# Kernel tuning notes

Measured on AMD Instinct MI355X. Metric: run time of the kernel, lower is better.

The kernel has to match this reference:

```python
import jax, jax.numpy as jnp
import numpy as np

L, H, HM, E = 2, 1024, 256, 64  # layers, hidden, hyper hidden, hyper embedding
B, T, D = 64, 256, 1024         # batch, time, input size (D == H so layers stack)


def setup_inputs() -> dict:
    key = jax.random.key(0)
    ks = jax.random.split(key, 16)
    n = jax.random.normal
    inp = {
        'x':   n(ks[0], (B, T, D), jnp.float32),
        # main LSTM weights: 4 gates (i,f,g,o); last dim is the input dim
        'Wx':  n(ks[1], (L, 4, H, D), jnp.float32) / np.sqrt(D),
        'Wh':  n(ks[2], (L, 4, H, H), jnp.float32) / np.sqrt(H),
        # hyper (meta) LSTM: input is concat(x_t, h) of size D+H
        'Wmx': n(ks[3], (L, 4 * HM, D + H), jnp.float32) / np.sqrt(D + H),
        'Wmh': n(ks[4], (L, 4 * HM, HM), jnp.float32) / np.sqrt(HM),
        'bm':  jnp.zeros((L, 4 * HM), jnp.float32),
        # hyper embeddings z per gate (hidden->4xE projections)
        'Wzx': n(ks[5], (L, HM, 4, E), jnp.float32) / np.sqrt(HM),
        'bzx': jnp.ones((L, 4, E), jnp.float32),
        'Wzh': n(ks[6], (L, HM, 4, E), jnp.float32) / np.sqrt(HM),
        'bzh': jnp.ones((L, 4, E), jnp.float32),
        'Wzb': n(ks[7], (L, HM, 4, E), jnp.float32) / np.sqrt(HM),
        # embedding -> per-unit modulation (E->H per gate)
        'Px':  n(ks[8], (L, 4, E, H), jnp.float32) / np.sqrt(E),
        'Ph':  n(ks[9], (L, 4, E, H), jnp.float32) / np.sqrt(E),
        'Pb':  n(ks[10], (L, 4, E, H), jnp.float32) / np.sqrt(E),
    }
    return inp


def _meta_lstm_forward(x, Wx, Wh, Wmx, Wmh, bm, Wzx, bzx, Wzh, bzh, Wzb, Px, Ph, Pb):
    Bb = x.shape[0]
    inp = x
    for l in range(L):
        def step(carry, xt, l=l):
            h, c, mh, mc = carry
            # hyper LSTM step on concat(x_t, h)
            xcat = jnp.concatenate([xt, h], axis=-1)
            mpre = xcat @ Wmx[l].T + mh @ Wmh[l].T + bm[l]
            mi, mf, mg, mo = jnp.split(mpre, 4, axis=-1)
            mc2 = jax.nn.sigmoid(mf) * mc + jax.nn.sigmoid(mi) * jnp.tanh(mg)
            mh2 = jax.nn.sigmoid(mo) * jnp.tanh(mc2)
            # gate embeddings and per-unit modulation vectors [B,4,H]
            zx = jnp.einsum('bm,mge->bge', mh2, Wzx[l]) + bzx[l]
            zh = jnp.einsum('bm,mge->bge', mh2, Wzh[l]) + bzh[l]
            zb = jnp.einsum('bm,mge->bge', mh2, Wzb[l])
            dx = jnp.einsum('bge,geh->bgh', zx, Px[l])
            dh = jnp.einsum('bge,geh->bgh', zh, Ph[l])
            db = jnp.einsum('bge,geh->bgh', zb, Pb[l])
            # main LSTM gate pre-activations, hyper-modulated
            gx = jnp.einsum('bd,ghd->bgh', xt, Wx[l])
            gh = jnp.einsum('bk,ghk->bgh', h, Wh[l])
            pre = dx * gx + dh * gh + db
            i_, f_, g_, o_ = pre[:, 0], pre[:, 1], pre[:, 2], pre[:, 3]
            c2 = jax.nn.sigmoid(f_) * c + jax.nn.sigmoid(i_) * jnp.tanh(g_)
            h2 = jax.nn.sigmoid(o_) * jnp.tanh(c2)
            return (h2, c2, mh2, mc2), h2
        init = (jnp.zeros((Bb, H), x.dtype), jnp.zeros((Bb, H), x.dtype),
                jnp.zeros((Bb, HM), x.dtype), jnp.zeros((Bb, HM), x.dtype))
        xs = jnp.swapaxes(inp, 0, 1)  # [T,B,D]
        _, hs = jax.lax.scan(step, init, xs)
        inp = jnp.swapaxes(hs, 0, 1)  # [B,T,H]
    return inp


def reference(x, Wx, Wh, Wmx, Wmh, bm, Wzx, bzx, Wzh, bzh, Wzb, Px, Ph, Pb):
    return _meta_lstm_forward(x, Wx, Wh, Wmx, Wmh, bm, Wzx, bzx, Wzh, bzh, Wzb, Px, Ph, Pb)
```

## Files before the change

kernel.cpp:

```cpp
#include <hip/hip_runtime.h>

#define Bb 64
#define Tt 256
#define Dd 1024
#define Hh 1024
#define HMm 256
#define Ee 64
#define DH 2048

__device__ __forceinline__ float b2f(unsigned short u){
    union{unsigned int i; float f;} v; v.i = ((unsigned int)u) << 16; return v.f;
}
__device__ __forceinline__ unsigned short f2bf(float f){
    union{float f; unsigned int i;} v; v.f = f;
    unsigned int x = v.i;
    unsigned int r = (x + 0x7fffu + ((x >> 16) & 1u)) >> 16;
    return (unsigned short)r;
}
__device__ __forceinline__ void up2(unsigned int u, float& lo, float& hi){
    union{unsigned int i; float f;} x, y;
    x.i = u << 16; y.i = u & 0xffff0000u; lo = x.f; hi = y.f;
}
__device__ __forceinline__ float sigf(float x){ return 1.f/(1.f + expf(-x)); }

__device__ __forceinline__ float dotT(const unsigned short* a, const unsigned short* w, float acc){
    uint4 ua = *(const uint4*)(const void*)a;
    uint4 uw = *(const uint4*)(const void*)w;
    float a0,a1,b0,b1;
    up2(ua.x,a0,a1); up2(uw.x,b0,b1); acc += a0*b0; acc += a1*b1;
    up2(ua.y,a0,a1); up2(uw.y,b0,b1); acc += a0*b0; acc += a1*b1;
    up2(ua.z,a0,a1); up2(uw.z,b0,b1); acc += a0*b0; acc += a1*b1;
    up2(ua.w,a0,a1); up2(uw.w,b0,b1); acc += a0*b0; acc += a1*b1;
    return acc;
}
__device__ __forceinline__ float dotT(const float* a, const unsigned short* w, float acc){
    float4 f0 = *(const float4*)(const void*)a;
    float4 f1 = *(const float4*)(const void*)(a+4);
    uint4 uw = *(const uint4*)(const void*)w;
    float b0,b1;
    up2(uw.x,b0,b1); acc += f0.x*b0; acc += f0.y*b1;
    up2(uw.y,b0,b1); acc += f0.z*b0; acc += f0.w*b1;
    up2(uw.z,b0,b1); acc += f1.x*b0; acc += f1.y*b1;
    up2(uw.w,b0,b1); acc += f1.z*b0; acc += f1.w*b1;
    return acc;
}
__device__ __forceinline__ float dotT(const float* a, const float* w, float acc){
    float4 a0 = *(const float4*)(const void*)a;
    float4 a1 = *(const float4*)(const void*)(a+4);
    float4 w0 = *(const float4*)(const void*)w;
    float4 w1 = *(const float4*)(const void*)(w+4);
    acc += a0.x*w0.x; acc += a0.y*w0.y; acc += a0.z*w0.z; acc += a0.w*w0.w;
    acc += a1.x*w1.x; acc += a1.y*w1.y; acc += a1.z*w1.z; acc += a1.w*w1.w;
    return acc;
}
__device__ __forceinline__ float ldT(const unsigned short* p){ return b2f(*p); }
__device__ __forceinline__ float ldT(const float* p){ return *p; }
__device__ __forceinline__ void stT(unsigned short* p, float v){ *p = f2bf(v); }
__device__ __forceinline__ void stT(float* p, float v){ *p = v; }

__global__ void k_detect(const unsigned short* __restrict__ x, int* __restrict__ flag){
    int tid = threadIdx.x;
    float v = fabsf(b2f(x[2 * tid]));
    bool in = (v > 1e-4f) && (v < 50.f);
    unsigned long long m = __ballot(in);
    if(tid == 0) *flag = (__popcll(m) >= 32) ? 0 : 1;
}

template<typename T>
__global__ __launch_bounds__(256) void k_meta(
    const T* __restrict__ xseq, int t,
    const float* __restrict__ hprev,
    const float* __restrict__ mhprev,
    float* __restrict__ mhnext,
    float* __restrict__ mc,
    const T* __restrict__ Wmx,
    const T* __restrict__ Wmh,
    const T* __restrict__ bm,
    float* __restrict__ xbuf,
    const int* __restrict__ flag)
{
    if(*flag != (int)(sizeof(T) == 4)) return;
    int tid = threadIdx.x;
    {
        int gid = blockIdx.x * 256 + tid;
        int xb = gid >> 10, xd = gid & 1023;
        xbuf[gid] = ldT(&xseq[((size_t)xb * Tt + t) * Dd + xd]);
    }
    int g  = tid & 3;
    int jj = (tid >> 2) & 3;
    int bb = tid >> 4;
    int j  = (blockIdx.x & 63) * 4 + jj;
    int b  = (blockIdx.x >> 6) * 16 + bb;
    int row = g * HMm + j;
    const T* xr  = xseq + ((size_t)b * Tt + t) * Dd;
    const T* wr  = Wmx + (size_t)row * DH;
    const T* wr2 = wr + Dd;
    const T* wm  = Wmh + (size_t)row * HMm;
    const float* hr = hprev + b * Hh;
    const float* mr = mhprev + b * HMm;
    float a0 = ldT(&bm[row]), a1 = 0.f, a2 = 0.f, a3 = 0.f;
    for(int d = 0; d < Dd; d += 32){
        a0 = dotT(xr+d,    wr+d,    a0);
        a1 = dotT(xr+d+8,  wr+d+8,  a1);
        a2 = dotT(xr+d+16, wr+d+16, a2);
        a3 = dotT(xr+d+24, wr+d+24, a3);
    }
    for(int k = 0; k < Hh; k += 32){
        a0 = dotT(hr+k,    wr2+k,    a0);
        a1 = dotT(hr+k+8,  wr2+k+8,  a1);
        a2 = dotT(hr+k+16, wr2+k+16, a2);
        a3 = dotT(hr+k+24, wr2+k+24, a3);
    }
    for(int m = 0; m < HMm; m += 32){
        a0 = dotT(mr+m,    wm+m,    a0);
        a1 = dotT(mr+m+8,  wm+m+8,  a1);
        a2 = dotT(mr+m+16, wm+m+16, a2);
        a3 = dotT(mr+m+24, wm+m+24, a3);
    }
    __shared__ float s[256];
    s[tid] = (a0 + a1) + (a2 + a3);
    __syncthreads();
    if(g == 0){
        float mi = s[tid], mf = s[tid+1], mg = s[tid+2], mo = s[tid+3];
        int idx = b * HMm + j;
        float mc2 = sigf(mf) * mc[idx] + sigf(mi) * tanhf(mg);
        mc[idx] = mc2;
        mhnext[idx] = sigf(mo) * tanhf(mc2);
    }
}

template<typename T>
__global__ __launch_bounds__(256) void k_z(
    const float* __restrict__ mh,
    const T* __restrict__ Wzx,
    const T* __restrict__ Wzh,
    const T* __restrict__ Wzb,
    const T* __restrict__ bzx,
    const T* __restrict__ bzh,
    float* __restrict__ z,
    const int* __restrict__ flag)
{
    if(*flag != (int)(sizeof(T) == 4)) return;
    int col = threadIdx.x;
    int b = blockIdx.x & 63;
    int s = blockIdx.x >> 6;
    const T* W = (s == 0) ? Wzx : ((s == 1) ? Wzh : Wzb);
    float acc = (s == 0) ? ldT(&bzx[col]) : ((s == 1) ? ldT(&bzh[col]) : 0.f);
    const float* mr = mh + b * HMm;
    #pragma unroll 8
    for(int m = 0; m < HMm; m++)
        acc += mr[m] * ldT(&W[m * 256 + col]);
    z[(size_t)(s * Bb + b) * 256 + col] = acc;
}

template<typename T>
__global__ __launch_bounds__(256) void k_main(
    const float* __restrict__ xbuf, int t,
    const float* __restrict__ hprev,
    float* __restrict__ hnext,
    float* __restrict__ c,
    const float* __restrict__ z,
    const T* __restrict__ Px,
    const T* __restrict__ Ph,
    const T* __restrict__ Pb,
    const T* __restrict__ Wx,
    const T* __restrict__ Wh,
    T* __restrict__ oseq,
    const int* __restrict__ flag)
{
    if(*flag != (int)(sizeof(T) == 4)) return;
    int tid = threadIdx.x;
    int hh = tid & 15, bb = tid >> 4;
    int h = (blockIdx.x & 63) * 16 + hh;
    int b = (blockIdx.x >> 6) * 16 + bb;
    const float* xr = xbuf + (size_t)b * Dd;
    const float* hr = hprev + b * Hh;
    const float* zxr = z + (size_t)b * 256;
    const float* zhr = z + (size_t)(Bb + b) * 256;
    const float* zbr = z + (size_t)(2 * Bb + b) * 256;
    float pre[4];
    #pragma unroll
    for(int g = 0; g < 4; g++){
        const T* wxr = Wx + ((size_t)g * Hh + h) * Dd;
        const T* whr = Wh + ((size_t)g * Hh + h) * Hh;
        float x0 = 0.f, x1 = 0.f, h0 = 0.f, h1 = 0.f;
        for(int d = 0; d < Dd; d += 16){
            x0 = dotT(xr+d,   wxr+d,   x0);
            x1 = dotT(xr+d+8, wxr+d+8, x1);
        }
        for(int k = 0; k < Hh; k += 16){
            h0 = dotT(hr+k,   whr+k,   h0);
            h1 = dotT(hr+k+8, whr+k+8, h1);
        }
        float gx = x0 + x1, gh = h0 + h1;
        const float* zx = zxr + g * Ee;
        const float* zh = zhr + g * Ee;
        const float* zb = zbr + g * Ee;
        float dx = 0.f, dh = 0.f, db = 0.f;
        #pragma unroll 8
        for(int e = 0; e < Ee; e++){
            int pi = (g * Ee + e) * Hh + h;
            dx += zx[e] * ldT(&Px[pi]);
            dh += zh[e] * ldT(&Ph[pi]);
            db += zb[e] * ldT(&Pb[pi]);
        }
        pre[g] = dx * gx + dh * gh + db;
    }
    int idx = b * Hh + h;
    float c2 = sigf(pre[1]) * c[idx] + sigf(pre[0]) * tanhf(pre[2]);
    float h2 = sigf(pre[3]) * tanhf(c2);
    c[idx] = c2;
    hnext[idx] = h2;
    stT(&oseq[((size_t)b * Tt + t) * Hh + h], h2);
}

#define LP(Ty, base, off) ((const Ty*)(base) + (off))

extern "C" void kernel_launch(void* const* d_in, const int* in_sizes, int n_in,
                              void* d_out, int out_size, void* d_ws, size_t ws_size,
                              hipStream_t stream) {
    (void)in_sizes; (void)n_in; (void)out_size; (void)ws_size;
    float* ws   = (float*)d_ws;
    float* h0   = ws;
    float* h1   = h0 + 65536;
    float* c    = h1 + 65536;
    float* mh0  = c  + 65536;
    float* mh1  = mh0 + 16384;
    float* mc   = mh1 + 16384;
    float* z    = mc  + 16384;
    float* xbuf = z   + 49152;
    int*   flag = (int*)(xbuf + 65536);

    k_detect<<<1, 64, 0, stream>>>((const unsigned short*)d_in[0], flag);

    for(int l = 0; l < 2; l++){
        hipMemsetAsync(ws, 0, (size_t)(3 * 65536 + 3 * 16384) * sizeof(float), stream);
        size_t oWx  = (size_t)l * 4 * Hh * Dd;
        size_t oWh  = (size_t)l * 4 * Hh * Hh;
        size_t oWmx = (size_t)l * 1024 * DH;
        size_t oWmh = (size_t)l * 1024 * HMm;
        size_t obm  = (size_t)l * 1024;
        size_t oWz  = (size_t)l * HMm * 256;
        size_t obz  = (size_t)l * 256;
        size_t oP   = (size_t)l * 4 * Ee * Hh;

        float *hp = h0, *hn = h1, *mp = mh0, *mn = mh1;
        for(int t = 0; t < Tt; t++){
            k_meta<unsigned short><<<256, 256, 0, stream>>>(
                LP(unsigned short, d_in[0], 0), t, hp, mp, mn, mc,
                LP(unsigned short, d_in[3], oWmx), LP(unsigned short, d_in[4], oWmh),
                LP(unsigned short, d_in[5], obm), xbuf, flag);
            k_meta<float><<<256, 256, 0, stream>>>(
                LP(float, d_in[0], 0), t, hp, mp, mn, mc,
                LP(float, d_in[3], oWmx), LP(float, d_in[4], oWmh),
                LP(float, d_in[5], obm), xbuf, flag);

            k_z<unsigned short><<<192, 256, 0, stream>>>(
                mn, LP(unsigned short, d_in[6], oWz), LP(unsigned short, d_in[8], oWz),
                LP(unsigned short, d_in[10], oWz), LP(unsigned short, d_in[7], obz),
                LP(unsigned short, d_in[9], obz), z, flag);
            k_z<float><<<192, 256, 0, stream>>>(
                mn, LP(float, d_in[6], oWz), LP(float, d_in[8], oWz),
                LP(float, d_in[10], oWz), LP(float, d_in[7], obz),
                LP(float, d_in[9], obz), z, flag);

            void* ov = (l == 0) ? (void*)d_in[0] : d_out;
            k_main<unsigned short><<<256, 256, 0, stream>>>(
                xbuf, t, hp, hn, c, z,
                LP(unsigned short, d_in[11], oP), LP(unsigned short, d_in[12], oP),
                LP(unsigned short, d_in[13], oP), LP(unsigned short, d_in[1], oWx),
                LP(unsigned short, d_in[2], oWh), (unsigned short*)ov, flag);
            k_main<float><<<256, 256, 0, stream>>>(
                xbuf, t, hp, hn, c, z,
                LP(float, d_in[11], oP), LP(float, d_in[12], oP),
                LP(float, d_in[13], oP), LP(float, d_in[1], oWx),
                LP(float, d_in[2], oWh), (float*)ov, flag);

            float* tmp = hp; hp = hn; hn = tmp;
            tmp = mp; mp = mn; mn = tmp;
        }
    }
}
```

Measured before the change: 244.4 ms.

## Fuse per-timestep kernels into one persistent cooperative kernel with grid syncs

Replaces the three per-timestep kernel launches (meta LSTM, z projection, main LSTM), each doubled for two dtype paths, with a single cooperative kernel per dtype. It loops over layers and timesteps internally and uses grid-wide syncs between stages. The main-gate stage is remapped so each thread computes four batch rows per weight row, reusing loaded weights in registers, and the meta stage is remapped to one hidden unit per block. The intent is to remove thousands of launches and improve weight reuse. In exchange it relies on cooperative launch residency and adds grid-sync latency at every stage.

```diff
diff --git a/kernel.cpp b/kernel.cpp
--- a/kernel.cpp
+++ b/kernel.cpp
@@ -1,4 +1,7 @@
 #include <hip/hip_runtime.h>
+#include <hip/hip_cooperative_groups.h>
+
+namespace cg = cooperative_groups;
 
 #define Bb 64
 #define Tt 256
@@ -6,7 +9,6 @@
 #define Hh 1024
 #define HMm 256
 #define Ee 64
-#define DH 2048
 
 __device__ __forceinline__ float b2f(unsigned short u){
     union{unsigned int i; float f;} v; v.i = ((unsigned int)u) << 16; return v.f;
@@ -23,40 +25,25 @@
 }
 __device__ __forceinline__ float sigf(float x){ return 1.f/(1.f + expf(-x)); }
 
-__device__ __forceinline__ float dotT(const unsigned short* a, const unsigned short* w, float acc){
-    uint4 ua = *(const uint4*)(const void*)a;
-    uint4 uw = *(const uint4*)(const void*)w;
-    float a0,a1,b0,b1;
-    up2(ua.x,a0,a1); up2(uw.x,b0,b1); acc += a0*b0; acc += a1*b1;
-    up2(ua.y,a0,a1); up2(uw.y,b0,b1); acc += a0*b0; acc += a1*b1;
-    up2(ua.z,a0,a1); up2(uw.z,b0,b1); acc += a0*b0; acc += a1*b1;
-    up2(ua.w,a0,a1); up2(uw.w,b0,b1); acc += a0*b0; acc += a1*b1;
-    return acc;
-}
-__device__ __forceinline__ float dotT(const float* a, const unsigned short* w, float acc){
-    float4 f0 = *(const float4*)(const void*)a;
-    float4 f1 = *(const float4*)(const void*)(a+4);
-    uint4 uw = *(const uint4*)(const void*)w;
-    float b0,b1;
-    up2(uw.x,b0,b1); acc += f0.x*b0; acc += f0.y*b1;
-    up2(uw.y,b0,b1); acc += f0.z*b0; acc += f0.w*b1;
-    up2(uw.z,b0,b1); acc += f1.x*b0; acc += f1.y*b1;
-    up2(uw.w,b0,b1); acc += f1.z*b0; acc += f1.w*b1;
-    return acc;
-}
-__device__ __forceinline__ float dotT(const float* a, const float* w, float acc){
-    float4 a0 = *(const float4*)(const void*)a;
-    float4 a1 = *(const float4*)(const void*)(a+4);
-    float4 w0 = *(const float4*)(const void*)w;
-    float4 w1 = *(const float4*)(const void*)(w+4);
-    acc += a0.x*w0.x; acc += a0.y*w0.y; acc += a0.z*w0.z; acc += a0.w*w0.w;
-    acc += a1.x*w1.x; acc += a1.y*w1.y; acc += a1.z*w1.z; acc += a1.w*w1.w;
-    return acc;
-}
 __device__ __forceinline__ float ldT(const unsigned short* p){ return b2f(*p); }
 __device__ __forceinline__ float ldT(const float* p){ return *p; }
 __device__ __forceinline__ void stT(unsigned short* p, float v){ *p = f2bf(v); }
 __device__ __forceinline__ void stT(float* p, float v){ *p = v; }
+
+__device__ __forceinline__ void ld8(const unsigned short* p, float* f){
+    uint4 u = *(const uint4*)(const void*)p;
+    up2(u.x,f[0],f[1]); up2(u.y,f[2],f[3]); up2(u.z,f[4],f[5]); up2(u.w,f[6],f[7]);
+}
+__device__ __forceinline__ void ld8(const float* p, float* f){
+    float4 a = *(const float4*)(const void*)p;
+    float4 b = *(const float4*)(const void*)(p+4);
+    f[0]=a.x; f[1]=a.y; f[2]=a.z; f[3]=a.w; f[4]=b.x; f[5]=b.y; f[6]=b.z; f[7]=b.w;
+}
+__device__ __forceinline__ float dot8(const float* a, const float* b, float acc){
+    #pragma unroll
+    for(int i=0;i<8;i++) acc += a[i]*b[i];
+    return acc;
+}
 
 __global__ void k_detect(const unsigned short* __restrict__ x, int* __restrict__ flag){
     int tid = threadIdx.x;
@@ -67,217 +54,205 @@
 }
 
 template<typename T>
-__global__ __launch_bounds__(256) void k_meta(
-    const T* __restrict__ xseq, int t,
-    const float* __restrict__ hprev,
-    const float* __restrict__ mhprev,
-    float* __restrict__ mhnext,
-    float* __restrict__ mc,
-    const T* __restrict__ Wmx,
-    const T* __restrict__ Wmh,
-    const T* __restrict__ bm,
-    float* __restrict__ xbuf,
-    const int* __restrict__ flag)
+__global__ __launch_bounds__(256) void coop_rnn(
+    const T* x,
+    const T* __restrict__ Wx, const T* __restrict__ Wh,
+    const T* __restrict__ Wmx, const T* __restrict__ Wmh, const T* __restrict__ bm,
+    const T* __restrict__ Wzx, const T* __restrict__ bzx,
+    const T* __restrict__ Wzh, const T* __restrict__ bzh, const T* __restrict__ Wzb,
+    const T* __restrict__ Px, const T* __restrict__ Ph, const T* __restrict__ Pb,
+    T* out, float* ws, const int* flag)
 {
     if(*flag != (int)(sizeof(T) == 4)) return;
-    int tid = threadIdx.x;
-    {
-        int gid = blockIdx.x * 256 + tid;
-        int xb = gid >> 10, xd = gid & 1023;
-        xbuf[gid] = ldT(&xseq[((size_t)xb * Tt + t) * Dd + xd]);
+    cg::grid_group grid = cg::this_grid();
+
+    float* h0   = ws;
+    float* h1   = ws + 65536;
+    float* cst  = ws + 131072;
+    float* m0   = ws + 196608;
+    float* m1   = ws + 212992;
+    float* mcst = ws + 229376;
+    float* z    = ws + 245760;
+    float* xbuf = ws + 294912;
+
+    int tid = threadIdx.x, bid = blockIdx.x;
+    int gid = bid * 256 + tid;
+
+    __shared__ float sA[256];
+    __shared__ float spre[1024];
+
+    for(int l = 0; l < 2; l++){
+        const T* xseq = l ? out : x;
+        const T* Wx_l  = Wx  + (size_t)l * 4194304;
+        const T* Wh_l  = Wh  + (size_t)l * 4194304;
+        const T* Wmx_l = Wmx + (size_t)l * 2097152;
+        const T* Wmh_l = Wmh + (size_t)l * 262144;
+        const T* bm_l  = bm  + l * 1024;
+        const T* Wz0 = Wzx + l * 65536;
+        const T* Wz1 = Wzh + l * 65536;
+        const T* Wz2 = Wzb + l * 65536;
+        const T* bz0 = bzx + l * 256;
+        const T* bz1 = bzh + l * 256;
+        const T* Px_l = Px + l * 262144;
+        const T* Ph_l = Ph + l * 262144;
+        const T* Pb_l = Pb + l * 262144;
+
+        h0[gid] = 0.f; cst[gid] = 0.f;
+        if(gid < 16384){ m0[gid] = 0.f; mcst[gid] = 0.f; }
+        float *hp = h0, *hn = h1, *mp = m0, *mn = m1;
+        grid.sync();
+
+        for(int t = 0; t < 256; t++){
+            {
+                int xb = gid >> 10, xd = gid & 1023;
+                xbuf[gid] = ldT(&xseq[((size_t)xb * Tt + t) * Dd + xd]);
+
+                int r = tid >> 6, b = tid & 63;
+                int row = r * 256 + bid;
+                const T* wr = Wmx_l + (size_t)row * 2048;
+                const T* wm = Wmh_l + (size_t)row * 256;
+                const T* xr = xseq + ((size_t)b * Tt + t) * Dd;
+                const float* hr = hp + b * 1024;
+                const float* mr = mp + b * 256;
+                float a0 = ldT(&bm_l[row]), a1 = 0.f, a2 = 0.f, a3 = 0.f;
+                float wf[8], vf[8];
+                for(int k = 0; k < 1024; k += 16){
+                    ld8(wr + k, wf);      ld8(xr + k, vf);      a0 = dot8(wf, vf, a0);
+                    ld8(wr + k + 8, wf);  ld8(xr + k + 8, vf);  a1 = dot8(wf, vf, a1);
+                }
+                for(int k = 0; k < 1024; k += 16){
+                    ld8(wr + 1024 + k, wf);     ld8(hr + k, vf);     a2 = dot8(wf, vf, a2);
+                    ld8(wr + 1024 + k + 8, wf); ld8(hr + k + 8, vf); a3 = dot8(wf, vf, a3);
+                }
+                for(int m = 0; m < 256; m += 16){
+                    ld8(wm + m, wf);     ld8(mr + m, vf);     a0 = dot8(wf, vf, a0);
+                    ld8(wm + m + 8, wf); ld8(mr + m + 8, vf); a1 = dot8(wf, vf, a1);
+                }
+                sA[tid] = (a0 + a1) + (a2 + a3);
+            }
+            __syncthreads();
+            if(tid < 64){
+                int b = tid;
+                float mi = sA[b], mf = sA[64 + b], mg = sA[128 + b], mo = sA[192 + b];
+                int idx = b * 256 + bid;
+                float mc2 = sigf(mf) * mcst[idx] + sigf(mi) * tanhf(mg);
+                mcst[idx] = mc2;
+                mn[idx] = sigf(mo) * tanhf(mc2);
+            }
+            grid.sync();
+
+            if(bid < 192){
+                int s_ = bid >> 6, b = bid & 63, col = tid;
+                const T* W = (s_ == 0) ? Wz0 : ((s_ == 1) ? Wz1 : Wz2);
+                float acc = (s_ == 0) ? ldT(&bz0[col]) : ((s_ == 1) ? ldT(&bz1[col]) : 0.f);
+                const float* mr = mn + b * 256;
+                #pragma unroll 8
+                for(int m = 0; m < 256; m++)
+                    acc += mr[m] * ldT(&W[m * 256 + col]);
+                z[(s_ * 64 + b) * 256 + col] = acc;
+            }
+            grid.sync();
+
+            {
+                int r16 = tid >> 4, bg = tid & 15;
+                int g = r16 >> 2, hh = r16 & 3;
+                int h = bid * 4 + hh;
+                int n = g * 1024 + h;
+                int b0 = bg * 4;
+                const T* wxr = Wx_l + (size_t)n * 1024;
+                const T* whr = Wh_l + (size_t)n * 1024;
+                float gx[4] = {0,0,0,0}, gh[4] = {0,0,0,0};
+                for(int k = 0; k < 1024; k += 8){
+                    float wf[8]; ld8(wxr + k, wf);
+                    #pragma unroll
+                    for(int i = 0; i < 4; i++){
+                        float xf[8]; ld8(xbuf + (b0 + i) * 1024 + k, xf);
+                        gx[i] = dot8(wf, xf, gx[i]);
+                    }
+                }
+                for(int k = 0; k < 1024; k += 8){
+                    float wf[8]; ld8(whr + k, wf);
+                    #pragma unroll
+                    for(int i = 0; i < 4; i++){
+                        float hf[8]; ld8(hp + (b0 + i) * 1024 + k, hf);
+                        gh[i] = dot8(wf, hf, gh[i]);
+                    }
+                }
+                float dx[4] = {0,0,0,0}, dh[4] = {0,0,0,0}, db[4] = {0,0,0,0};
+                for(int e = 0; e < 64; e++){
+                    int pi = (g * 64 + e) * 1024 + h;
+                    float pxv = ldT(&Px_l[pi]);
+                    float phv = ldT(&Ph_l[pi]);
+                    float pbv = ldT(&Pb_l[pi]);
+                    int zc = g * 64 + e;
+                    #pragma unroll
+                    for(int i = 0; i < 4; i++){
+                        int b = b0 + i;
+                        dx[i] += z[(b) * 256 + zc] * pxv;
+                        dh[i] += z[(64 + b) * 256 + zc] * phv;
+                        db[i] += z[(128 + b) * 256 + zc] * pbv;
+                    }
+                }
+                #pragma unroll
+                for(int i = 0; i < 4; i++)
+                    spre[(g * 4 + hh) * 64 + b0 + i] = dx[i] * gx[i] + dh[i] * gh[i] + db[i];
+            }
+            __syncthreads();
+            {
+                int hh = tid >> 6, b = tid & 63;
+                float pi_ = spre[(0 * 4 + hh) * 64 + b];
+                float pf_ = spre[(1 * 4 + hh) * 64 + b];
+                float pg_ = spre[(2 * 4 + hh) * 64 + b];
+                float po_ = spre[(3 * 4 + hh) * 64 + b];
+                int h = bid * 4 + hh;
+                int idx = b * 1024 + h;
+                float c2 = sigf(pf_) * cst[idx] + sigf(pi_) * tanhf(pg_);
+                float h2 = sigf(po_) * tanhf(c2);
+                cst[idx] = c2;
+                hn[idx] = h2;
+                stT(&out[((size_t)b * Tt + t) * Dd + h], h2);
+            }
+            grid.sync();
+
+            float* tp = hp; hp = hn; hn = tp;
+            tp = mp; mp = mn; mn = tp;
+        }
     }
-    int g  = tid & 3;
-    int jj = (tid >> 2) & 3;
-    int bb = tid >> 4;
-    int j  = (blockIdx.x & 63) * 4 + jj;
-    int b  = (blockIdx.x >> 6) * 16 + bb;
-    int row = g * HMm + j;
-    const T* xr  = xseq + ((size_t)b * Tt + t) * Dd;
-    const T* wr  = Wmx + (size_t)row * DH;
-    const T* wr2 = wr + Dd;
-    const T* wm  = Wmh + (size_t)row * HMm;
-    const float* hr = hprev + b * Hh;
-    const float* mr = mhprev + b * HMm;
-    float a0 = ldT(&bm[row]), a1 = 0.f, a2 = 0.f, a3 = 0.f;
-    for(int d = 0; d < Dd; d += 32){
-        a0 = dotT(xr+d,    wr+d,    a0);
-        a1 = dotT(xr+d+8,  wr+d+8,  a1);
-        a2 = dotT(xr+d+16, wr+d+16, a2);
-        a3 = dotT(xr+d+24, wr+d+24, a3);
-    }
-    for(int k = 0; k < Hh; k += 32){
-        a0 = dotT(hr+k,    wr2+k,    a0);
-        a1 = dotT(hr+k+8,  wr2+k+8,  a1);
-        a2 = dotT(hr+k+16, wr2+k+16, a2);
-        a3 = dotT(hr+k+24, wr2+k+24, a3);
-    }
-    for(int m = 0; m < HMm; m += 32){
-        a0 = dotT(mr+m,    wm+m,    a0);
-        a1 = dotT(mr+m+8,  wm+m+8,  a1);
-        a2 = dotT(mr+m+16, wm+m+16, a2);
-        a3 = dotT(mr+m+24, wm+m+24, a3);
-    }
-    __shared__ float s[256];
-    s[tid] = (a0 + a1) + (a2 + a3);
-    __syncthreads();
-    if(g == 0){
-        float mi = s[tid], mf = s[tid+1], mg = s[tid+2], mo = s[tid+3];
-        int idx = b * HMm + j;
-        float mc2 = sigf(mf) * mc[idx] + sigf(mi) * tanhf(mg);
-        mc[idx] = mc2;
-        mhnext[idx] = sigf(mo) * tanhf(mc2);
-    }
 }
 
 template<typename T>
-__global__ __launch_bounds__(256) void k_z(
-    const float* __restrict__ mh,
-    const T* __restrict__ Wzx,
-    const T* __restrict__ Wzh,
-    const T* __restrict__ Wzb,
-    const T* __restrict__ bzx,
-    const T* __restrict__ bzh,
-    float* __restrict__ z,
-    const int* __restrict__ flag)
-{
-    if(*flag != (int)(sizeof(T) == 4)) return;
-    int col = threadIdx.x;
-    int b = blockIdx.x & 63;
-    int s = blockIdx.x >> 6;
-    const T* W = (s == 0) ? Wzx : ((s == 1) ? Wzh : Wzb);
-    float acc = (s == 0) ? ldT(&bzx[col]) : ((s == 1) ? ldT(&bzh[col]) : 0.f);
-    const float* mr = mh + b * HMm;
-    #pragma unroll 8
-    for(int m = 0; m < HMm; m++)
-        acc += mr[m] * ldT(&W[m * 256 + col]);
-    z[(size_t)(s * Bb + b) * 256 + col] = acc;
-}
-
-template<typename T>
-__global__ __launch_bounds__(256) void k_main(
-    const float* __restrict__ xbuf, int t,
-    const float* __restrict__ hprev,
-    float* __restrict__ hnext,
-    float* __restrict__ c,
-    const float* __restrict__ z,
-    const T* __restrict__ Px,
-    const T* __restrict__ Ph,
-    const T* __restrict__ Pb,
-    const T* __restrict__ Wx,
-    const T* __restrict__ Wh,
-    T* __restrict__ oseq,
-    const int* __restrict__ flag)
-{
-    if(*flag != (int)(sizeof(T) == 4)) return;
-    int tid = threadIdx.x;
-    int hh = tid & 15, bb = tid >> 4;
-    int h = (blockIdx.x & 63) * 16 + hh;
-    int b = (blockIdx.x >> 6) * 16 + bb;
-    const float* xr = xbuf + (size_t)b * Dd;
-    const float* hr = hprev + b * Hh;
-    const float* zxr = z + (size_t)b * 256;
-    const float* zhr = z + (size_t)(Bb + b) * 256;
-    const float* zbr = z + (size_t)(2 * Bb + b) * 256;
-    float pre[4];
-    #pragma unroll
-    for(int g = 0; g < 4; g++){
-        const T* wxr = Wx + ((size_t)g * Hh + h) * Dd;
-        const T* whr = Wh + ((size_t)g * Hh + h) * Hh;
-        float x0 = 0.f, x1 = 0.f, h0 = 0.f, h1 = 0.f;
-        for(int d = 0; d < Dd; d += 16){
-            x0 = dotT(xr+d,   wxr+d,   x0);
-            x1 = dotT(xr+d+8, wxr+d+8, x1);
-        }
-        for(int k = 0; k < Hh; k += 16){
-            h0 = dotT(hr+k,   whr+k,   h0);
-            h1 = dotT(hr+k+8, whr+k+8, h1);
-        }
-        float gx = x0 + x1, gh = h0 + h1;
-        const float* zx = zxr + g * Ee;
-        const float* zh = zhr + g * Ee;
-        const float* zb = zbr + g * Ee;
-        float dx = 0.f, dh = 0.f, db = 0.f;
-        #pragma unroll 8
-        for(int e = 0; e < Ee; e++){
-            int pi = (g * Ee + e) * Hh + h;
-            dx += zx[e] * ldT(&Px[pi]);
-            dh += zh[e] * ldT(&Ph[pi]);
-            db += zb[e] * ldT(&Pb[pi]);
-        }
-        pre[g] = dx * gx + dh * gh + db;
-    }
-    int idx = b * Hh + h;
-    float c2 = sigf(pre[1]) * c[idx] + sigf(pre[0]) * tanhf(pre[2]);
-    float h2 = sigf(pre[3]) * tanhf(c2);
-    c[idx] = c2;
-    hnext[idx] = h2;
-    stT(&oseq[((size_t)b * Tt + t) * Hh + h], h2);
-}
-
-#define LP(Ty, base, off) ((const Ty*)(base) + (off))
+static void launch_path(void* const* d_in, void* d_out, float* ws, int* flag, hipStream_t stream){
+    const T* xp   = (const T*)d_in[0];
+    const T* Wxp  = (const T*)d_in[1];
+    const T* Whp  = (const T*)d_in[2];
+    const T* Wmxp = (const T*)d_in[3];
+    const T* Wmhp = (const T*)d_in[4];
+    const T* bmp  = (const T*)d_in[5];
+    const T* Wzxp = (const T*)d_in[6];
+    const T* bzxp = (const T*)d_in[7];
+    const T* Wzhp = (const T*)d_in[8];
+    const T* bzhp = (const T*)d_in[9];
+    const T* Wzbp = (const T*)d_in[10];
+    const T* Pxp  = (const T*)d_in[11];
+    const T* Php  = (const T*)d_in[12];
+    const T* Pbp  = (const T*)d_in[13];
+    T* outp = (T*)d_out;
+    void* args[] = {
+        (void*)&xp, (void*)&Wxp, (void*)&Whp, (void*)&Wmxp, (void*)&Wmhp, (void*)&bmp,
+        (void*)&Wzxp, (void*)&bzxp, (void*)&Wzhp, (void*)&bzhp, (void*)&Wzbp,
+        (void*)&Pxp, (void*)&Php, (void*)&Pbp, (void*)&outp, (void*)&ws, (void*)&flag
+    };
+    hipLaunchCooperativeKernel((void*)coop_rnn<T>, dim3(256), dim3(256), args, 0, stream);
+}
 
 extern "C" void kernel_launch(void* const* d_in, const int* in_sizes, int n_in,
                               void* d_out, int out_size, void* d_ws, size_t ws_size,
                               hipStream_t stream) {
     (void)in_sizes; (void)n_in; (void)out_size; (void)ws_size;
-    float* ws   = (float*)d_ws;
-    float* h0   = ws;
-    float* h1   = h0 + 65536;
-    float* c    = h1 + 65536;
-    float* mh0  = c  + 65536;
-    float* mh1  = mh0 + 16384;
-    float* mc   = mh1 + 16384;
-    float* z    = mc  + 16384;
-    float* xbuf = z   + 49152;
-    int*   flag = (int*)(xbuf + 65536);
+    float* ws = (float*)d_ws;
+    int* flag = (int*)(ws + 360448);
 
     k_detect<<<1, 64, 0, stream>>>((const unsigned short*)d_in[0], flag);
-
-    for(int l = 0; l < 2; l++){
-        hipMemsetAsync(ws, 0, (size_t)(3 * 65536 + 3 * 16384) * sizeof(float), stream);
-        size_t oWx  = (size_t)l * 4 * Hh * Dd;
-        size_t oWh  = (size_t)l * 4 * Hh * Hh;
-        size_t oWmx = (size_t)l * 1024 * DH;
-        size_t oWmh = (size_t)l * 1024 * HMm;
-        size_t obm  = (size_t)l * 1024;
-        size_t oWz  = (size_t)l * HMm * 256;
-        size_t obz  = (size_t)l * 256;
-        size_t oP   = (size_t)l * 4 * Ee * Hh;
-
-        float *hp = h0, *hn = h1, *mp = mh0, *mn = mh1;
-        for(int t = 0; t < Tt; t++){
-            k_meta<unsigned short><<<256, 256, 0, stream>>>(
-                LP(unsigned short, d_in[0], 0), t, hp, mp, mn, mc,
-                LP(unsigned short, d_in[3], oWmx), LP(unsigned short, d_in[4], oWmh),
-                LP(unsigned short, d_in[5], obm), xbuf, flag);
-            k_meta<float><<<256, 256, 0, stream>>>(
-                LP(float, d_in[0], 0), t, hp, mp, mn, mc,
-                LP(float, d_in[3], oWmx), LP(float, d_in[4], oWmh),
-                LP(float, d_in[5], obm), xbuf, flag);
-
-            k_z<unsigned short><<<192, 256, 0, stream>>>(
-                mn, LP(unsigned short, d_in[6], oWz), LP(unsigned short, d_in[8], oWz),
-                LP(unsigned short, d_in[10], oWz), LP(unsigned short, d_in[7], obz),
-                LP(unsigned short, d_in[9], obz), z, flag);
-            k_z<float><<<192, 256, 0, stream>>>(
-                mn, LP(float, d_in[6], oWz), LP(float, d_in[8], oWz),
-                LP(float, d_in[10], oWz), LP(float, d_in[7], obz),
-                LP(float, d_in[9], obz), z, flag);
-
-            void* ov = (l == 0) ? (void*)d_in[0] : d_out;
-            k_main<unsigned short><<<256, 256, 0, stream>>>(
-                xbuf, t, hp, hn, c, z,
-                LP(unsigned short, d_in[11], oP), LP(unsigned short, d_in[12], oP),
-                LP(unsigned short, d_in[13], oP), LP(unsigned short, d_in[1], oWx),
-                LP(unsigned short, d_in[2], oWh), (unsigned short*)ov, flag);
-            k_main<float><<<256, 256, 0, stream>>>(
-                xbuf, t, hp, hn, c, z,
-                LP(float, d_in[11], oP), LP(float, d_in[12], oP),
-                LP(float, d_in[13], oP), LP(float, d_in[1], oWx),
-                LP(float, d_in[2], oWh), (float*)ov, flag);
-
-            float* tmp = hp; hp = hn; hn = tmp;
-            tmp = mp; mp = mn; mn = tmp;
-        }
-    }
-}
+    launch_path<unsigned short>(d_in, d_out, ws, flag, stream);
+    launch_path<float>(d_in, d_out, ws, flag, stream);
+}
```

Result: faster. 236.9 ms (-3.1%).
